# Kernel tuning notes

Hardware: AMD Instinct MI355X
Metric: run time of the kernel (lower is better)

Reference implementation:

```python
import jax, jax.numpy as jnp
import numpy as np

B, T, S = 128, 512, 30      # batch, input temporal length, sensor channels
F_NUM, KS, NL = 64, 5, 4    # conv filters, kernel size, n conv layers
H, NC = 128, 18             # GRU hidden dim, n classes


def setup_inputs() -> dict:
    key = jax.random.key(0)
    ks = jax.random.split(key, 16)
    r = lambda i, shape, s=0.05: (jax.random.normal(ks[i], shape, jnp.float32) * s)
    return {
        "x": jax.random.normal(ks[0], (B, 1, T, S), jnp.float32),
        "conv0_w": r(1, (F_NUM, 1, KS, 1), 0.2),          # first Conv2d (in=1)
        "convs_w": r(2, (3, F_NUM, F_NUM, KS, 1), 0.05),  # conv layers 1..3
        "conv_b": r(3, (NL, F_NUM)),
        "bn_gamma": jnp.ones((NL, F_NUM), jnp.float32),
        "bn_beta": jnp.zeros((NL, F_NUM), jnp.float32),
        "bn_mean": jnp.zeros((NL, F_NUM), jnp.float32),
        "bn_var": jnp.ones((NL, F_NUM), jnp.float32),
        "wq": r(4, (F_NUM, F_NUM), 0.1),
        "wk": r(5, (F_NUM, F_NUM), 0.1),
        "wv": r(6, (F_NUM, F_NUM), 0.1),
        "sa_gamma": jnp.array([0.1], jnp.float32),
        "fc1_w": r(7, (H, S * F_NUM), 0.02),
        "fc1_b": r(8, (H,)),
        "gru_wih": r(9, (2, 3 * H, H), 0.05),
        "gru_whh": r(10, (2, 3 * H, H), 0.05),
        "gru_bih": r(11, (2, 3 * H)),
        "gru_bhh": r(12, (2, 3 * H)),
        "pred_w": r(13, (NC, H), 0.05),
        "pred_b": r(14, (NC,)),
    }


def reference(x, conv0_w, convs_w, conv_b, bn_gamma, bn_beta, bn_mean, bn_var,
              wq, wk, wv, sa_gamma, fc1_w, fc1_b,
              gru_wih, gru_whh, gru_bih, gru_bhh, pred_w, pred_b):
    eps = 1e-5

    def conv_relu_bn(y, w, b, g, be, m, v):
        # Conv2d kernel (KS,1) stride (2,1), then ReLU, then BatchNorm (eval mode)
        y = jax.lax.conv_general_dilated(
            y, w, (2, 1), 'VALID',
            dimension_numbers=('NCHW', 'OIHW', 'NCHW')) + b[None, :, None, None]
        y = jax.nn.relu(y)
        inv = g / jnp.sqrt(v + eps)
        return y * inv[None, :, None, None] + (be - m * inv)[None, :, None, None]

    x = conv_relu_bn(x, conv0_w, conv_b[0], bn_gamma[0], bn_beta[0], bn_mean[0], bn_var[0])
    for i in range(3):  # fixed small layer loop
        x = conv_relu_bn(x, convs_w[i], conv_b[i + 1], bn_gamma[i + 1],
                         bn_beta[i + 1], bn_mean[i + 1], bn_var[i + 1])

    Bn, Fn, Ln, Sn = x.shape
    # Fold time into batch: per-timestep SelfAttention over (F, S) slices, vectorized
    xs = jnp.transpose(x, (0, 2, 1, 3)).reshape(Bn * Ln, Fn, Sn)  # (N, F, S)
    f = jnp.einsum('of,nfs->nos', wq, xs)   # query (1x1 conv1d, no bias)
    g = jnp.einsum('of,nfs->nos', wk, xs)   # key
    h = jnp.einsum('of,nfs->nos', wv, xs)   # value
    scores = jnp.einsum('noi,noj->nij', f, g)         # bmm(f^T, g): (N, S, S)
    beta = jax.nn.softmax(scores, axis=1)             # softmax over dim=1 (as torch)
    o = sa_gamma[0] * jnp.einsum('nfi,nij->nfj', h, beta) + xs  # (N, F, S)

    # cat over t then permute(0,3,1,2).reshape == (B, L, F*S)
    seq = o.reshape(Bn, Ln, Fn * Sn)
    seq = jax.nn.relu(seq @ fc1_w.T + fc1_b)          # (B, L, H); dropout = eval noop
    xs_t = jnp.transpose(seq, (1, 0, 2))              # (L, B, H) seq-first for GRU

    def gru_layer(xseq, wih, whh, bih, bhh):
        Hd = whh.shape[1]
        def step(hprev, xt):
            gi = xt @ wih.T + bih
            gh = hprev @ whh.T + bhh
            ir, iz, inn = jnp.split(gi, 3, axis=-1)
            hr, hz, hn = jnp.split(gh, 3, axis=-1)
            r = jax.nn.sigmoid(ir + hr)
            z = jax.nn.sigmoid(iz + hz)
            n = jnp.tanh(inn + r * hn)
            hnew = (1.0 - z) * n + z * hprev
            return hnew, hnew
        h0 = jnp.zeros((xseq.shape[1], Hd), xseq.dtype)
        _, ys = jax.lax.scan(step, h0, xseq)
        return ys

    for l in range(2):  # 2-layer GRU (inter-layer dropout = eval noop)
        xs_t = gru_layer(xs_t, gru_wih[l], gru_whh[l], gru_bih[l], gru_bhh[l])

    return xs_t[-1] @ pred_w.T + pred_b               # (B, NC)
```

## Files before the change

kernel.cpp:

```cpp
#include <hip/hip_runtime.h>
#include <math.h>

#define EPS 1e-5f

#define B_  128
#define T0_ 512
#define S_  30
#define F_  64
#define L1_ 254
#define L2_ 125
#define L3_ 61
#define L4_ 29
#define BS_ (B_*S_)
#define N_  (B_*L4_)
#define H_  128
#define NC_ 18
#define KFS 1920

typedef __attribute__((ext_vector_type(8))) short short8;
typedef __attribute__((ext_vector_type(16))) float f32x16;

__device__ __forceinline__ uint32_t f2bf(float f) {
    uint32_t u = __float_as_uint(f);
    return (u + 0x7fffu + ((u >> 16) & 1u)) >> 16;
}

typedef const __attribute__((address_space(1))) uint32_t* gas_t;
typedef __attribute__((address_space(3))) uint32_t* las_t;
__device__ __forceinline__ void glds16(const void* g, void* l) {
    __builtin_amdgcn_global_load_lds((gas_t)g, (las_t)l, 16, 0, 0);
}

#define MFMA(a,b,c) __builtin_amdgcn_mfma_f32_32x32x16_bf16(a, b, c, 0, 0, 0)

__global__ __launch_bounds__(256) void prepack_kernel(
    const float* __restrict__ wcs, ushort* __restrict__ aw)
{
    int i = blockIdx.x*256 + threadIdx.x;
    int l = i / 20480, r = i - l*20480;
    int j = r & 7, f = (r >> 3) & 63, g = r >> 9;
    int chalf = g & 1, ck = (g >> 1) & 3, kh = g >> 3;
    int c = ck*16 + chalf*8 + j;
    float w = wcs[l*20480 + f*320 + c*5 + kh];
    uint32_t h = f2bf(w);
    uint32_t lo = f2bf(w - __uint_as_float(h << 16));
    aw[l*40960 + r]         = (ushort)h;
    aw[l*40960 + 20480 + r] = (ushort)lo;
}

__device__ __forceinline__ f32x16 conv_mm(
    const ushort* __restrict__ Ash, const ushort* __restrict__ Bh,
    const ushort* __restrict__ Bl, int f0, int t0, int tcol, int chalf)
{
    f32x16 acc;
    #pragma unroll
    for (int i = 0; i < 16; i++) acc[i] = 0.f;
    int fa = (f0 + tcol)*8;
    int t = t0 + tcol;
    #pragma unroll
    for (int kh = 0; kh < 5; kh++) {
        int tp = 2*t + kh;
        int sw = (tp >> 3) & 7;
        const ushort* brh = Bh + tp*64;
        const ushort* brl = Bl + tp*64;
        #pragma unroll
        for (int ck = 0; ck < 4; ck++) {
            int g = (kh*4+ck)*2 + chalf;
            short8 AH = *(const short8*)(Ash + g*512 + fa);
            short8 AL = *(const short8*)(Ash + 20480 + g*512 + fa);
            int col = (((ck*2+chalf) ^ sw) << 3);
            short8 BH = *(const short8*)(brh + col);
            short8 BL = *(const short8*)(brl + col);
            acc = MFMA(AH, BH, acc);
            acc = MFMA(AH, BL, acc);
            acc = MFMA(AL, BH, acc);
        }
    }
    return acc;
}

__global__ __launch_bounds__(512) void conv01_mfma(
    const float* __restrict__ x,  const float* __restrict__ w0,
    const ushort* __restrict__ aw, const float* __restrict__ cb,
    const float* __restrict__ bg, const float* __restrict__ bb,
    const float* __restrict__ bm, const float* __restrict__ bv,
    char* __restrict__ y1h, char* __restrict__ y1l)
{
    __shared__ uint32_t Ash_w[20480];
    __shared__ ushort Yt[2][264*64];
    __shared__ float xl[T0_];
    int bs = blockIdx.x, b = bs/S_, s = bs - b*S_;
    int tid = threadIdx.x;
    #pragma unroll
    for (int k = 0; k < 10; k++)
        glds16((const char*)aw + k*8192 + tid*16, (char*)Ash_w + k*8192 + (tid>>6)*1024);
    xl[tid] = x[(b*T0_ + tid)*S_ + s];
    __syncthreads();
    {
        int c = tid & 63;
        float w00=w0[c*5], w01=w0[c*5+1], w02=w0[c*5+2], w03=w0[c*5+3], w04=w0[c*5+4];
        float bias = cb[c];
        float inv = bg[c]*rsqrtf(bv[c]+EPS);
        float add = bb[c]-bm[c]*inv;
        for (int tp = (tid>>6); tp < 264; tp += 8) {
            float val = 0.f;
            if (tp < L1_) {
                float a = bias + w00*xl[2*tp] + w01*xl[2*tp+1] + w02*xl[2*tp+2]
                               + w03*xl[2*tp+3] + w04*xl[2*tp+4];
                val = fmaxf(a, 0.f)*inv + add;
            }
            uint32_t h = f2bf(val);
            uint32_t l = f2bf(val - __uint_as_float(h<<16));
            int col = c ^ ((tp>>3 & 7) << 3);
            Yt[0][tp*64 + col] = (ushort)h;
            Yt[1][tp*64 + col] = (ushort)l;
        }
    }
    __syncthreads();
    int lane = tid & 63, wv = tid >> 6;
    int tcol = lane & 31, chalf = lane >> 5;
    int f0 = (wv>>2)*32, t0 = (wv&3)*32;
    f32x16 acc = conv_mm((const ushort*)Ash_w, Yt[0], Yt[1], f0, t0, tcol, chalf);
    __syncthreads();
    int t = t0 + tcol;
    if (t < L2_) {
        int swzo = ((t>>1) ^ (t>>3)) & 7;
        #pragma unroll
        for (int rq = 0; rq < 4; rq++) {
            int fb = f0 + 8*rq + 4*chalf;
            uint32_t h[4], l[4];
            #pragma unroll
            for (int j = 0; j < 4; j++) {
                int r = rq*4 + j, f = fb + j;
                float inv = bg[64+f]*rsqrtf(bv[64+f]+EPS);
                float val = fmaxf(acc[r]+cb[64+f], 0.f)*inv + (bb[64+f]-bm[64+f]*inv);
                h[j] = f2bf(val);
                l[j] = f2bf(val - __uint_as_float(h[j]<<16));
            }
            int pos = ((((fb>>3) ^ swzo) << 3) + (fb & 7));
            uint2 H; H.x = h[0] | (h[1]<<16); H.y = h[2] | (h[3]<<16);
            uint2 L; L.x = l[0] | (l[1]<<16); L.y = l[2] | (l[3]<<16);
            *(uint2*)&Yt[0][t*64 + pos] = H;
            *(uint2*)&Yt[1][t*64 + pos] = L;
        }
    }
    __syncthreads();
    for (int i = tid; i < 2000; i += 512) {
        int pl = i >= 1000, jj = pl ? i-1000 : i;
        int tr = jj >> 3, p = jj & 7;
        int q = p ^ ((tr>>1) & 7);
        uint4 v = *(const uint4*)&Yt[pl][tr*64 + q*8];
        *(uint4*)((pl ? y1l : y1h) + (size_t)bs*16000 + tr*128 + p*16) = v;
    }
}

__global__ __launch_bounds__(512) void conv2_mfma(
    const ushort* __restrict__ aw, const float* __restrict__ cb,
    const float* __restrict__ bg, const float* __restrict__ bb,
    const float* __restrict__ bm, const float* __restrict__ bv,
    char* __restrict__ yh, char* __restrict__ yl)
{
    __shared__ uint32_t Ash_w[20480];
    __shared__ ushort Yt[2][2][132*64];
    int bs0 = blockIdx.x*2, tid = threadIdx.x;
    const char* asrc = (const char*)aw + 81920;
    #pragma unroll
    for (int k = 0; k < 10; k++)
        glds16(asrc + k*8192 + tid*16, (char*)Ash_w + k*8192 + (tid>>6)*1024);
    #pragma unroll
    for (int sl = 0; sl < 2; sl++)
        #pragma unroll
        for (int pl = 0; pl < 2; pl++) {
            const char* src = (pl ? yl : yh) + (size_t)(bs0+sl)*16000;
            glds16(src + tid*16,        (char*)&Yt[sl][pl][0] + (tid>>6)*1024);
            glds16(src + 8192 + tid*16, (char*)&Yt[sl][pl][0] + 8192 + (tid>>6)*1024);
        }
    __syncthreads();
    for (int i = tid; i < 4*224; i += 512) {
        int g = i / 224, w2 = i - g*224;
        ((uint32_t*)&Yt[g>>1][g&1][125*64])[w2] = 0;
    }
    __syncthreads();
    int lane = tid & 63, wv = tid >> 6;
    int tcol = lane & 31, chalf = lane >> 5;
    int sl = wv >> 2, f0 = ((wv>>1)&1)*32, t0 = (wv&1)*32;
    f32x16 acc = conv_mm((const ushort*)Ash_w, Yt[sl][0], Yt[sl][1], f0, t0, tcol, chalf);
    __syncthreads();
    int t = t0 + tcol;
    if (t < L3_) {
        int swzo = ((t>>1) ^ (t>>3)) & 7;
        #pragma unroll
        for (int rq = 0; rq < 4; rq++) {
            int fb = f0 + 8*rq + 4*chalf;
            uint32_t h[4], l[4];
            #pragma unroll
            for (int j = 0; j < 4; j++) {
                int r = rq*4 + j, f = fb + j;
                float inv = bg[128+f]*rsqrtf(bv[128+f]+EPS);
                float val = fmaxf(acc[r]+cb[128+f], 0.f)*inv + (bb[128+f]-bm[128+f]*inv);
                h[j] = f2bf(val);
                l[j] = f2bf(val - __uint_as_float(h[j]<<16));
            }
            int pos = ((((fb>>3) ^ swzo) << 3) + (fb & 7));
            uint2 H; H.x = h[0] | (h[1]<<16); H.y = h[2] | (h[3]<<16);
            uint2 L; L.x = l[0] | (l[1]<<16); L.y = l[2] | (l[3]<<16);
            *(uint2*)&Yt[sl][0][t*64 + pos] = H;
            *(uint2*)&Yt[sl][1][t*64 + pos] = L;
        }
    }
    __syncthreads();
    for (int i = tid; i < 1952; i += 512) {
        int s2 = i / 976, r2 = i - s2*976;
        int pl = r2 >= 488, jj = pl ? r2-488 : r2;
        int tr = jj >> 3, p = jj & 7;
        int q = p ^ ((tr>>1) & 7);
        uint4 v = *(const uint4*)&Yt[s2][pl][tr*64 + q*8];
        *(uint4*)((pl ? yl : yh) + (size_t)(bs0+s2)*16000 + tr*128 + p*16) = v;
    }
}

__global__ __launch_bounds__(512) void conv3_mfma(
    const ushort* __restrict__ aw, const float* __restrict__ cb,
    const float* __restrict__ bg, const float* __restrict__ bb,
    const float* __restrict__ bm, const float* __restrict__ bv,
    const char* __restrict__ yh, const char* __restrict__ yl,
    float* __restrict__ y3)
{
    __shared__ uint32_t Ash_w[20480];
    __shared__ ushort Yt[4][2][68*64];
    int bs0 = blockIdx.x*4, tid = threadIdx.x;
    const char* asrc = (const char*)aw + 163840;
    #pragma unroll
    for (int k = 0; k < 10; k++)
        glds16(asrc + k*8192 + tid*16, (char*)Ash_w + k*8192 + (tid>>6)*1024);
    #pragma unroll
    for (int sl = 0; sl < 4; sl++)
        #pragma unroll
        for (int pl = 0; pl < 2; pl++) {
            const char* src = (pl ? yl : yh) + (size_t)(bs0+sl)*16000;
            glds16(src + tid*16, (char*)&Yt[sl][pl][0] + (tid>>6)*1024);
        }
    __syncthreads();
    for (int i = tid; i < 8*224; i += 512) {
        int g = i / 224, w2 = i - g*224;
        ((uint32_t*)&Yt[g>>1][g&1][61*64])[w2] = 0;
    }
    __syncthreads();
    int lane = tid & 63, wv = tid >> 6;
    int tcol = lane & 31, chalf = lane >> 5;
    int sl = wv >> 1, f0 = (wv&1)*32;
    f32x16 acc = conv_mm((const ushort*)Ash_w, Yt[sl][0], Yt[sl][1], f0, 0, tcol, chalf);
    int t = tcol;
    if (t < L4_) {
        #pragma unroll
        for (int r = 0; r < 16; r++) {
            int f = f0 + (r&3) + 8*(r>>2) + 4*chalf;
            float inv = bg[192+f]*rsqrtf(bv[192+f]+EPS);
            float val = fmaxf(acc[r]+cb[192+f], 0.f)*inv + (bb[192+f]-bm[192+f]*inv);
            y3[((size_t)(bs0+sl)*F_ + f)*L4_ + t] = val;
        }
    }
}

__global__ __launch_bounds__(256) void transp_kernel(
    const float* __restrict__ y3, float* __restrict__ xs)
{
    __shared__ float tl[15*F_*L4_];
    int b = blockIdx.x >> 1, s0 = (blockIdx.x & 1)*15;
    int tid = threadIdx.x;
    const float* src = y3 + (b*S_ + s0)*F_*L4_;
    for (int i = tid; i < 15*F_*L4_; i += 256) tl[i] = src[i];
    __syncthreads();
    for (int i = tid; i < L4_*F_*15; i += 256) {
        int l = i/(F_*15), f = (i/15)%F_, ss = i%15;
        xs[((b*L4_+l)*F_+f)*S_ + s0+ss] = tl[(ss*F_+f)*L4_ + l];
    }
}

__global__ __launch_bounds__(256) void attn_kernel(
    const float* __restrict__ xsg, const float* __restrict__ wq,
    const float* __restrict__ wk,  const float* __restrict__ wv,
    const float* __restrict__ gam, float* __restrict__ seq)
{
    __shared__ float X[F_][32];
    __shared__ float QKV[192][36];
    __shared__ float BETA[S_][36];
    int n = blockIdx.x, tid = threadIdx.x;
    for (int i = tid; i < KFS; i += 256) X[i/S_][i%S_] = xsg[n*KFS + i];
    for (int i = tid; i < 128; i += 256) X[i>>1][30 + (i&1)] = 0.f;
    __syncthreads();

    if (tid < 192) {
        int wsel = tid >> 6, row = tid & 63;
        const float* W = (wsel==0) ? wq : (wsel==1) ? wk : wv;
        float4 wr_[16];
        #pragma unroll
        for (int u = 0; u < 16; u++) wr_[u] = ((const float4*)(W + row*64))[u];
        float acc[32];
        #pragma unroll
        for (int i = 0; i < 32; i++) acc[i] = 0.f;
        #pragma unroll
        for (int u = 0; u < 16; u++) {
            float4 w4 = wr_[u];
            #pragma unroll
            for (int c = 0; c < 4; c++) {
                float wv_ = (c==0) ? w4.x : (c==1) ? w4.y : (c==2) ? w4.z : w4.w;
                const float4* xr = (const float4*)&X[u*4+c][0];
                #pragma unroll
                for (int q = 0; q < 8; q++) {
                    float4 xq = xr[q];
                    acc[q*4+0] += wv_*xq.x; acc[q*4+1] += wv_*xq.y;
                    acc[q*4+2] += wv_*xq.z; acc[q*4+3] += wv_*xq.w;
                }
            }
        }
        #pragma unroll
        for (int q = 0; q < 8; q++) {
            float4 o4; o4.x=acc[q*4]; o4.y=acc[q*4+1]; o4.z=acc[q*4+2]; o4.w=acc[q*4+3];
            *(float4*)&QKV[tid][q*4] = o4;
        }
    }
    __syncthreads();

    if (tid < 240) {
        int j = tid >> 3, iq = tid & 7;
        float4 s4 = {0.f, 0.f, 0.f, 0.f};
        for (int o = 0; o < 64; o++) {
            float4 q4 = *(const float4*)&QKV[o][iq*4];
            float kv = QKV[64+o][j];
            s4.x += q4.x*kv; s4.y += q4.y*kv; s4.z += q4.z*kv; s4.w += q4.w*kv;
        }
        if (iq == 7) { s4.z = -1e30f; s4.w = -1e30f; }
        float m = fmaxf(fmaxf(s4.x, s4.y), fmaxf(s4.z, s4.w));
        m = fmaxf(m, __shfl_xor(m, 1, 8));
        m = fmaxf(m, __shfl_xor(m, 2, 8));
        m = fmaxf(m, __shfl_xor(m, 4, 8));
        float e0 = expf(s4.x-m), e1 = expf(s4.y-m), e2 = expf(s4.z-m), e3 = expf(s4.w-m);
        if (iq == 7) { e2 = 0.f; e3 = 0.f; }
        float sum = e0+e1+e2+e3;
        sum += __shfl_xor(sum, 1, 8);
        sum += __shfl_xor(sum, 2, 8);
        sum += __shfl_xor(sum, 4, 8);
        float inv = 1.f/sum;
        int i0 = iq*4;
        BETA[i0][j]   = e0*inv;
        BETA[i0+1][j] = e1*inv;
        if (iq < 7) { BETA[i0+2][j] = e2*inv; BETA[i0+3][j] = e3*inv; }
    }
    __syncthreads();

    {
        int f = tid >> 2, jh = tid & 3;
        float acc[8];
        #pragma unroll
        for (int i = 0; i < 8; i++) acc[i] = 0.f;
        for (int i = 0; i < S_; i++) {
            float v = QKV[128+f][i];
            float4 b0 = *(const float4*)&BETA[i][jh*8];
            float4 b1 = *(const float4*)&BETA[i][jh*8+4];
            acc[0] += v*b0.x; acc[1] += v*b0.y; acc[2] += v*b0.z; acc[3] += v*b0.w;
            acc[4] += v*b1.x; acc[5] += v*b1.y; acc[6] += v*b1.z; acc[7] += v*b1.w;
        }
        float g = gam[0];
        int j0 = jh*8;
        #pragma unroll
        for (int jj = 0; jj < 8; jj++) {
            int j = j0 + jj;
            if (j < S_) seq[n*KFS + f*S_ + j] = g*acc[jj] + X[f][j];
        }
    }
}

__global__ __launch_bounds__(256) void fc1_kernel(
    const float* __restrict__ seq, const float* __restrict__ w,
    const float* __restrict__ bias, float* __restrict__ out)
{
    __shared__ float Sm[8*KFS];
    int n0 = blockIdx.x*8, tid = threadIdx.x;
    for (int i = tid; i < 8*KFS; i += 256) Sm[i] = seq[n0*KFS + i];
    __syncthreads();
    int h = tid & 127, rp = tid >> 7;
    float acc[4] = {0,0,0,0};
    const float4* wp = (const float4*)(w + h*KFS);
    #pragma unroll 4
    for (int k = 0; k < KFS/4; k++) {
        float4 wvv = wp[k];
        #pragma unroll
        for (int j = 0; j < 4; j++) {
            float4 sv = ((const float4*)&Sm[(rp*4+j)*KFS])[k];
            acc[j] += wvv.x*sv.x + wvv.y*sv.y + wvv.z*sv.z + wvv.w*sv.w;
        }
    }
    float bb2 = bias[h];
    #pragma unroll
    for (int j = 0; j < 4; j++)
        out[(n0 + rp*4 + j)*H_ + h] = fmaxf(acc[j] + bb2, 0.f);
}

__global__ __launch_bounds__(768) void gru_kernel(
    const float* __restrict__ xin,  const float* __restrict__ wih,
    const float* __restrict__ whh,  const float* __restrict__ bih,
    const float* __restrict__ bhh,  const float* __restrict__ pw,
    const float* __restrict__ pb,   float* __restrict__ out)
{
    __shared__ float xh[H_], hh[H_], gi[3*H_], gh[3*H_], ys[L4_][H_];
    int b = blockIdx.x, tid = threadIdx.x;
    int mat = tid / 384, j = tid % 384;
    float4 wr[32];
    for (int layer = 0; layer < 2; layer++) {
        const float* wsrc = (mat ? whh : wih) + layer*384*128 + j*128;
        #pragma unroll
        for (int u = 0; u < 32; u++) wr[u] = ((const float4*)wsrc)[u];
        float bias = (mat ? bhh : bih)[layer*384 + j];
        if (tid < H_) hh[tid] = 0.f;
        __syncthreads();
        for (int t = 0; t < L4_; t++) {
            if (tid < H_) xh[tid] = (layer == 0) ? xin[(b*L4_+t)*H_ + tid] : ys[t][tid];
            __syncthreads();
            const float* src = mat ? hh : xh;
            float a0=0,a1=0,a2=0,a3=0;
            #pragma unroll
            for (int u = 0; u < 32; u++) {
                float4 xv = ((const float4*)src)[u];
                a0 += wr[u].x*xv.x; a1 += wr[u].y*xv.y;
                a2 += wr[u].z*xv.z; a3 += wr[u].w*xv.w;
            }
            float g = (a0+a1)+(a2+a3) + bias;
            if (mat) gh[j] = g; else gi[j] = g;
            __syncthreads();
            if (tid < H_) {
                int m = tid;
                float r = 1.f/(1.f+expf(-(gi[m]      + gh[m])));
                float z = 1.f/(1.f+expf(-(gi[m+128]  + gh[m+128])));
                float n = tanhf(gi[m+256] + r*gh[m+256]);
                float hnew = (1.f-z)*n + z*hh[m];
                hh[m] = hnew; ys[t][m] = hnew;
            }
            __syncthreads();
        }
    }
    if (tid < NC_) {
        float a = pb[tid];
        for (int k = 0; k < H_; k++) a += pw[tid*H_+k]*hh[k];
        out[b*NC_ + tid] = a;
    }
}

extern "C" void kernel_launch(void* const* d_in, const int* in_sizes, int n_in,
                              void* d_out, int out_size, void* d_ws, size_t ws_size,
                              hipStream_t stream) {
    const float* x    = (const float*)d_in[0];
    const float* w0   = (const float*)d_in[1];
    const float* wcs  = (const float*)d_in[2];
    const float* cb   = (const float*)d_in[3];
    const float* bg   = (const float*)d_in[4];
    const float* bb   = (const float*)d_in[5];
    const float* bm   = (const float*)d_in[6];
    const float* bv   = (const float*)d_in[7];
    const float* wq   = (const float*)d_in[8];
    const float* wk   = (const float*)d_in[9];
    const float* wv   = (const float*)d_in[10];
    const float* gam  = (const float*)d_in[11];
    const float* fw   = (const float*)d_in[12];
    const float* fb   = (const float*)d_in[13];
    const float* gwih = (const float*)d_in[14];
    const float* gwhh = (const float*)d_in[15];
    const float* gbih = (const float*)d_in[16];
    const float* gbhh = (const float*)d_in[17];
    const float* pw   = (const float*)d_in[18];
    const float* pb   = (const float*)d_in[19];
    float* out = (float*)d_out;
    uint32_t* wsu = (uint32_t*)d_ws;

    ushort* aw  = (ushort*)wsu;
    char* y1h   = (char*)(wsu + 61440);
    char* y1l   = (char*)(wsu + 15425536);
    float* y3v  = (float*)(wsu + 30789632);
    float* seqv = (float*)(wsu + 30789632);
    float* xsv  = (float*)(wsu + 37916672);
    float* f1v  = (float*)(wsu + 37916672);

    prepack_kernel<<<240, 256, 0, stream>>>(wcs, aw);
    conv01_mfma<<<BS_, 512, 0, stream>>>(x, w0, aw, cb, bg, bb, bm, bv, y1h, y1l);
    conv2_mfma<<<BS_/2, 512, 0, stream>>>(aw, cb, bg, bb, bm, bv, y1h, y1l);
    conv3_mfma<<<BS_/4, 512, 0, stream>>>(aw, cb, bg, bb, bm, bv, y1h, y1l, y3v);
    transp_kernel<<<2*B_, 256, 0, stream>>>(y3v, xsv);
    attn_kernel<<<N_, 256, 0, stream>>>(xsv, wq, wk, wv, gam, seqv);
    fc1_kernel<<<N_/8, 256, 0, stream>>>(seqv, fw, fb, f1v);
    gru_kernel<<<B_, 768, 0, stream>>>(f1v, gwih, gwhh, gbih, gbhh, pw, pb, out);
}
```

Measured before the change: 720.0 us.

## Keep conv weights in registers and loop persistent blocks over multiple slices

The three MFMA conv kernels now load their bf16 hi/lo weight fragments once into registers instead of staging 80KB of weights in LDS per block. Each block then processes several (b,s) slices: 5 for conv01, 8 for conv2 and conv3, with double-buffered async global-to-LDS loads of the next slices in conv2 and conv3. BN epilogue constants are precomputed into shared memory, and the first-layer conv is vectorised over 4 channels per thread. The aim is to amortise weight loads and free LDS for 2 blocks per CU. The cost is high register pressure from 40 short8 fragments per thread, which could cause spills, and fewer blocks in the grid.

```diff
diff --git a/kernel.cpp b/kernel.cpp
--- a/kernel.cpp
+++ b/kernel.cpp
@@ -33,6 +33,8 @@
 
 #define MFMA(a,b,c) __builtin_amdgcn_mfma_f32_32x32x16_bf16(a, b, c, 0, 0, 0)
 
+union ABu { uint4 u; short8 s; };
+
 __global__ __launch_bounds__(256) void prepack_kernel(
     const float* __restrict__ wcs, ushort* __restrict__ aw)
 {
@@ -48,15 +50,26 @@
     aw[l*40960 + 20480 + r] = (ushort)lo;
 }
 
-__device__ __forceinline__ f32x16 conv_mm(
-    const ushort* __restrict__ Ash, const ushort* __restrict__ Bh,
-    const ushort* __restrict__ Bl, int f0, int t0, int tcol, int chalf)
+__device__ __forceinline__ void load_areg(const ushort* __restrict__ aw_l,
+                                          int f0, int tcol, int chalf,
+                                          ABu* AH_, ABu* AL_)
+{
+    #pragma unroll
+    for (int idx = 0; idx < 20; idx++) {
+        int r = (idx*2 + chalf)*512 + (f0 + tcol)*8;
+        AH_[idx].u = *(const uint4*)(aw_l + r);
+        AL_[idx].u = *(const uint4*)(aw_l + 20480 + r);
+    }
+}
+
+__device__ __forceinline__ f32x16 conv_mm_reg(
+    const ABu* AH_, const ABu* AL_,
+    const ushort* __restrict__ Bh, const ushort* __restrict__ Bl,
+    int t, int chalf)
 {
     f32x16 acc;
     #pragma unroll
     for (int i = 0; i < 16; i++) acc[i] = 0.f;
-    int fa = (f0 + tcol)*8;
-    int t = t0 + tcol;
     #pragma unroll
     for (int kh = 0; kh < 5; kh++) {
         int tp = 2*t + kh;
@@ -65,200 +78,276 @@
         const ushort* brl = Bl + tp*64;
         #pragma unroll
         for (int ck = 0; ck < 4; ck++) {
-            int g = (kh*4+ck)*2 + chalf;
-            short8 AH = *(const short8*)(Ash + g*512 + fa);
-            short8 AL = *(const short8*)(Ash + 20480 + g*512 + fa);
-            int col = (((ck*2+chalf) ^ sw) << 3);
+            int idx = kh*4 + ck;
+            int col = (((ck*2 + chalf) ^ sw) << 3);
             short8 BH = *(const short8*)(brh + col);
             short8 BL = *(const short8*)(brl + col);
-            acc = MFMA(AH, BH, acc);
-            acc = MFMA(AH, BL, acc);
-            acc = MFMA(AL, BH, acc);
+            acc = MFMA(AH_[idx].s, BH, acc);
+            acc = MFMA(AH_[idx].s, BL, acc);
+            acc = MFMA(AL_[idx].s, BH, acc);
         }
     }
     return acc;
 }
 
-__global__ __launch_bounds__(512) void conv01_mfma(
+__global__ __launch_bounds__(512, 2) void conv01_mfma(
     const float* __restrict__ x,  const float* __restrict__ w0,
     const ushort* __restrict__ aw, const float* __restrict__ cb,
     const float* __restrict__ bg, const float* __restrict__ bb,
     const float* __restrict__ bm, const float* __restrict__ bv,
     char* __restrict__ y1h, char* __restrict__ y1l)
 {
-    __shared__ uint32_t Ash_w[20480];
     __shared__ ushort Yt[2][264*64];
     __shared__ float xl[T0_];
-    int bs = blockIdx.x, b = bs/S_, s = bs - b*S_;
+    __shared__ float ep0[64], ep1[64], ep2[64];
     int tid = threadIdx.x;
-    #pragma unroll
-    for (int k = 0; k < 10; k++)
-        glds16((const char*)aw + k*8192 + tid*16, (char*)Ash_w + k*8192 + (tid>>6)*1024);
-    xl[tid] = x[(b*T0_ + tid)*S_ + s];
-    __syncthreads();
-    {
-        int c = tid & 63;
-        float w00=w0[c*5], w01=w0[c*5+1], w02=w0[c*5+2], w03=w0[c*5+3], w04=w0[c*5+4];
-        float bias = cb[c];
-        float inv = bg[c]*rsqrtf(bv[c]+EPS);
-        float add = bb[c]-bm[c]*inv;
-        for (int tp = (tid>>6); tp < 264; tp += 8) {
-            float val = 0.f;
-            if (tp < L1_) {
-                float a = bias + w00*xl[2*tp] + w01*xl[2*tp+1] + w02*xl[2*tp+2]
-                               + w03*xl[2*tp+3] + w04*xl[2*tp+4];
-                val = fmaxf(a, 0.f)*inv + add;
-            }
-            uint32_t h = f2bf(val);
-            uint32_t l = f2bf(val - __uint_as_float(h<<16));
-            int col = c ^ ((tp>>3 & 7) << 3);
-            Yt[0][tp*64 + col] = (ushort)h;
-            Yt[1][tp*64 + col] = (ushort)l;
-        }
-    }
-    __syncthreads();
     int lane = tid & 63, wv = tid >> 6;
     int tcol = lane & 31, chalf = lane >> 5;
-    int f0 = (wv>>2)*32, t0 = (wv&3)*32;
-    f32x16 acc = conv_mm((const ushort*)Ash_w, Yt[0], Yt[1], f0, t0, tcol, chalf);
-    __syncthreads();
-    int t = t0 + tcol;
-    if (t < L2_) {
-        int swzo = ((t>>1) ^ (t>>3)) & 7;
-        #pragma unroll
-        for (int rq = 0; rq < 4; rq++) {
-            int fb = f0 + 8*rq + 4*chalf;
-            uint32_t h[4], l[4];
-            #pragma unroll
-            for (int j = 0; j < 4; j++) {
-                int r = rq*4 + j, f = fb + j;
-                float inv = bg[64+f]*rsqrtf(bv[64+f]+EPS);
-                float val = fmaxf(acc[r]+cb[64+f], 0.f)*inv + (bb[64+f]-bm[64+f]*inv);
-                h[j] = f2bf(val);
-                l[j] = f2bf(val - __uint_as_float(h[j]<<16));
-            }
-            int pos = ((((fb>>3) ^ swzo) << 3) + (fb & 7));
-            uint2 H; H.x = h[0] | (h[1]<<16); H.y = h[2] | (h[3]<<16);
-            uint2 L; L.x = l[0] | (l[1]<<16); L.y = l[2] | (l[3]<<16);
-            *(uint2*)&Yt[0][t*64 + pos] = H;
-            *(uint2*)&Yt[1][t*64 + pos] = L;
-        }
-    }
-    __syncthreads();
-    for (int i = tid; i < 2000; i += 512) {
-        int pl = i >= 1000, jj = pl ? i-1000 : i;
-        int tr = jj >> 3, p = jj & 7;
-        int q = p ^ ((tr>>1) & 7);
-        uint4 v = *(const uint4*)&Yt[pl][tr*64 + q*8];
-        *(uint4*)((pl ? y1l : y1h) + (size_t)bs*16000 + tr*128 + p*16) = v;
-    }
-}
-
-__global__ __launch_bounds__(512) void conv2_mfma(
+    int f0 = (wv>>2)*32, t0 = (wv&3)*32, t = t0 + tcol;
+
+    ABu AH_[20], AL_[20];
+    load_areg(aw, f0, tcol, chalf, AH_, AL_);
+
+    int cq = tid & 15, tpb = tid >> 4, c0 = cq*4;
+    float w0r[20], inv0[4], add0[4], b0r[4];
+    #pragma unroll
+    for (int j = 0; j < 4; j++) {
+        int c = c0 + j;
+        #pragma unroll
+        for (int u = 0; u < 5; u++) w0r[j*5+u] = w0[c*5+u];
+        float iv = bg[c]*rsqrtf(bv[c]+EPS);
+        inv0[j] = iv; add0[j] = bb[c]-bm[c]*iv; b0r[j] = cb[c];
+    }
+    if (tid < 64) {
+        float iv = bg[64+tid]*rsqrtf(bv[64+tid]+EPS);
+        ep0[tid] = iv; ep1[tid] = bb[64+tid]-bm[64+tid]*iv; ep2[tid] = cb[64+tid];
+    }
+
+    for (int sl = 0; sl < 5; sl++) {
+        int bs = blockIdx.x*5 + sl, b = bs/S_, s = bs - b*S_;
+        xl[tid] = x[(b*T0_ + tid)*S_ + s];
+        __syncthreads();
+        #pragma unroll
+        for (int k = 0; k < 9; k++) {
+            int tp = tpb + k*32;
+            if (tp < 264) {
+                float v4[4];
+                if (tp < L1_) {
+                    float2 xa = *(const float2*)&xl[2*tp];
+                    float2 xb = *(const float2*)&xl[2*tp+2];
+                    float2 xc = *(const float2*)&xl[2*tp+4];
+                    #pragma unroll
+                    for (int j = 0; j < 4; j++) {
+                        float a = b0r[j] + w0r[j*5]*xa.x + w0r[j*5+1]*xa.y
+                                + w0r[j*5+2]*xb.x + w0r[j*5+3]*xb.y + w0r[j*5+4]*xc.x;
+                        v4[j] = fmaxf(a, 0.f)*inv0[j] + add0[j];
+                    }
+                } else { v4[0]=v4[1]=v4[2]=v4[3]=0.f; }
+                uint32_t h0=f2bf(v4[0]), h1=f2bf(v4[1]), h2=f2bf(v4[2]), h3=f2bf(v4[3]);
+                uint2 H; H.x = h0|(h1<<16); H.y = h2|(h3<<16);
+                uint2 L;
+                L.x = f2bf(v4[0]-__uint_as_float(h0<<16)) | (f2bf(v4[1]-__uint_as_float(h1<<16))<<16);
+                L.y = f2bf(v4[2]-__uint_as_float(h2<<16)) | (f2bf(v4[3]-__uint_as_float(h3<<16))<<16);
+                int pos = tp*64 + (c0 ^ (((tp>>3)&7)<<3));
+                *(uint2*)&Yt[0][pos] = H;
+                *(uint2*)&Yt[1][pos] = L;
+            }
+        }
+        __syncthreads();
+        f32x16 acc = conv_mm_reg(AH_, AL_, Yt[0], Yt[1], t, chalf);
+        __syncthreads();
+        if (t < L2_) {
+            int swzo = ((t>>1) ^ (t>>3)) & 7;
+            #pragma unroll
+            for (int rq = 0; rq < 4; rq++) {
+                int fb = f0 + 8*rq + 4*chalf;
+                uint32_t h[4], l[4];
+                #pragma unroll
+                for (int j = 0; j < 4; j++) {
+                    int r = rq*4 + j, f = fb + j;
+                    float val = fmaxf(acc[r]+ep2[f], 0.f)*ep0[f] + ep1[f];
+                    h[j] = f2bf(val);
+                    l[j] = f2bf(val - __uint_as_float(h[j]<<16));
+                }
+                int pos = ((((fb>>3) ^ swzo) << 3) + (fb & 7));
+                uint2 H; H.x = h[0] | (h[1]<<16); H.y = h[2] | (h[3]<<16);
+                uint2 L; L.x = l[0] | (l[1]<<16); L.y = l[2] | (l[3]<<16);
+                *(uint2*)&Yt[0][t*64 + pos] = H;
+                *(uint2*)&Yt[1][t*64 + pos] = L;
+            }
+        }
+        __syncthreads();
+        for (int i = tid; i < 2000; i += 512) {
+            int pl = i >= 1000, jj = pl ? i-1000 : i;
+            int tr = jj >> 3, p = jj & 7;
+            int q = p ^ ((tr>>1) & 7);
+            uint4 v = *(const uint4*)&Yt[pl][tr*64 + q*8];
+            *(uint4*)((pl ? y1l : y1h) + (size_t)bs*16000 + tr*128 + p*16) = v;
+        }
+    }
+}
+
+__global__ __launch_bounds__(512, 2) void conv2_mfma(
     const ushort* __restrict__ aw, const float* __restrict__ cb,
     const float* __restrict__ bg, const float* __restrict__ bb,
     const float* __restrict__ bm, const float* __restrict__ bv,
     char* __restrict__ yh, char* __restrict__ yl)
 {
-    __shared__ uint32_t Ash_w[20480];
-    __shared__ ushort Yt[2][2][132*64];
-    int bs0 = blockIdx.x*2, tid = threadIdx.x;
-    const char* asrc = (const char*)aw + 81920;
-    #pragma unroll
-    for (int k = 0; k < 10; k++)
-        glds16(asrc + k*8192 + tid*16, (char*)Ash_w + k*8192 + (tid>>6)*1024);
-    #pragma unroll
-    for (int sl = 0; sl < 2; sl++)
-        #pragma unroll
-        for (int pl = 0; pl < 2; pl++) {
-            const char* src = (pl ? yl : yh) + (size_t)(bs0+sl)*16000;
-            glds16(src + tid*16,        (char*)&Yt[sl][pl][0] + (tid>>6)*1024);
-            glds16(src + 8192 + tid*16, (char*)&Yt[sl][pl][0] + 8192 + (tid>>6)*1024);
-        }
-    __syncthreads();
-    for (int i = tid; i < 4*224; i += 512) {
-        int g = i / 224, w2 = i - g*224;
-        ((uint32_t*)&Yt[g>>1][g&1][125*64])[w2] = 0;
-    }
-    __syncthreads();
+    __shared__ ushort Yt[2][2][2][132*64];
+    __shared__ float ep0[64], ep1[64], ep2[64];
+    int tid = threadIdx.x;
     int lane = tid & 63, wv = tid >> 6;
     int tcol = lane & 31, chalf = lane >> 5;
-    int sl = wv >> 2, f0 = ((wv>>1)&1)*32, t0 = (wv&1)*32;
-    f32x16 acc = conv_mm((const ushort*)Ash_w, Yt[sl][0], Yt[sl][1], f0, t0, tcol, chalf);
-    __syncthreads();
-    int t = t0 + tcol;
-    if (t < L3_) {
-        int swzo = ((t>>1) ^ (t>>3)) & 7;
-        #pragma unroll
-        for (int rq = 0; rq < 4; rq++) {
-            int fb = f0 + 8*rq + 4*chalf;
-            uint32_t h[4], l[4];
-            #pragma unroll
-            for (int j = 0; j < 4; j++) {
-                int r = rq*4 + j, f = fb + j;
-                float inv = bg[128+f]*rsqrtf(bv[128+f]+EPS);
-                float val = fmaxf(acc[r]+cb[128+f], 0.f)*inv + (bb[128+f]-bm[128+f]*inv);
-                h[j] = f2bf(val);
-                l[j] = f2bf(val - __uint_as_float(h[j]<<16));
-            }
-            int pos = ((((fb>>3) ^ swzo) << 3) + (fb & 7));
-            uint2 H; H.x = h[0] | (h[1]<<16); H.y = h[2] | (h[3]<<16);
-            uint2 L; L.x = l[0] | (l[1]<<16); L.y = l[2] | (l[3]<<16);
-            *(uint2*)&Yt[sl][0][t*64 + pos] = H;
-            *(uint2*)&Yt[sl][1][t*64 + pos] = L;
-        }
-    }
-    __syncthreads();
-    for (int i = tid; i < 1952; i += 512) {
-        int s2 = i / 976, r2 = i - s2*976;
-        int pl = r2 >= 488, jj = pl ? r2-488 : r2;
-        int tr = jj >> 3, p = jj & 7;
-        int q = p ^ ((tr>>1) & 7);
-        uint4 v = *(const uint4*)&Yt[s2][pl][tr*64 + q*8];
-        *(uint4*)((pl ? yl : yh) + (size_t)(bs0+s2)*16000 + tr*128 + p*16) = v;
-    }
-}
-
-__global__ __launch_bounds__(512) void conv3_mfma(
+    int slw = wv >> 2, f0 = ((wv>>1)&1)*32, t0 = (wv&1)*32, t = t0 + tcol;
+    int blk = blockIdx.x;
+
+    ABu AH_[20], AL_[20];
+    load_areg(aw + 40960, f0, tcol, chalf, AH_, AL_);
+    if (tid < 64) {
+        float iv = bg[128+tid]*rsqrtf(bv[128+tid]+EPS);
+        ep0[tid] = iv; ep1[tid] = bb[128+tid]-bm[128+tid]*iv; ep2[tid] = cb[128+tid];
+    }
+    #pragma unroll
+    for (int sl2 = 0; sl2 < 2; sl2++)
+        #pragma unroll
+        for (int pl = 0; pl < 2; pl++) {
+            const char* src = (pl ? yl : yh) + (size_t)(blk*8 + sl2)*16000;
+            glds16(src + tid*16,        (char*)&Yt[0][sl2][pl][0] + (tid>>6)*1024);
+            glds16(src + 8192 + tid*16, (char*)&Yt[0][sl2][pl][0] + 8192 + (tid>>6)*1024);
+        }
+    for (int i = tid; i < 1024; i += 512) {
+        int g = i >> 7, w2 = i & 127;
+        ((uint32_t*)&Yt[g>>2][(g>>1)&1][g&1][128*64])[w2] = 0;
+    }
+    __syncthreads();
+    for (int i = tid; i < 384; i += 512) {
+        int g = i / 96, w2 = i - g*96;
+        ((uint32_t*)&Yt[0][g>>1][g&1][125*64])[w2] = 0;
+    }
+    __syncthreads();
+
+    for (int it = 0; it < 4; it++) {
+        int buf = it & 1;
+        int bs0 = blk*8 + it*2;
+        if (it < 3) {
+            #pragma unroll
+            for (int sl2 = 0; sl2 < 2; sl2++)
+                #pragma unroll
+                for (int pl = 0; pl < 2; pl++) {
+                    const char* src = (pl ? yl : yh) + (size_t)(bs0 + 2 + sl2)*16000;
+                    glds16(src + tid*16,        (char*)&Yt[buf^1][sl2][pl][0] + (tid>>6)*1024);
+                    glds16(src + 8192 + tid*16, (char*)&Yt[buf^1][sl2][pl][0] + 8192 + (tid>>6)*1024);
+                }
+        }
+        f32x16 acc = conv_mm_reg(AH_, AL_, Yt[buf][slw][0], Yt[buf][slw][1], t, chalf);
+        __syncthreads();
+        if (it < 3) {
+            for (int i = tid; i < 384; i += 512) {
+                int g = i / 96, w2 = i - g*96;
+                ((uint32_t*)&Yt[buf^1][g>>1][g&1][125*64])[w2] = 0;
+            }
+        }
+        if (t < L3_) {
+            int swzo = ((t>>1) ^ (t>>3)) & 7;
+            #pragma unroll
+            for (int rq = 0; rq < 4; rq++) {
+                int fb = f0 + 8*rq + 4*chalf;
+                uint32_t h[4], l[4];
+                #pragma unroll
+                for (int j = 0; j < 4; j++) {
+                    int r = rq*4 + j, f = fb + j;
+                    float val = fmaxf(acc[r]+ep2[f], 0.f)*ep0[f] + ep1[f];
+                    h[j] = f2bf(val);
+                    l[j] = f2bf(val - __uint_as_float(h[j]<<16));
+                }
+                int pos = ((((fb>>3) ^ swzo) << 3) + (fb & 7));
+                uint2 H; H.x = h[0] | (h[1]<<16); H.y = h[2] | (h[3]<<16);
+                uint2 L; L.x = l[0] | (l[1]<<16); L.y = l[2] | (l[3]<<16);
+                *(uint2*)&Yt[buf][slw][0][t*64 + pos] = H;
+                *(uint2*)&Yt[buf][slw][1][t*64 + pos] = L;
+            }
+        }
+        __syncthreads();
+        for (int i = tid; i < 1952; i += 512) {
+            int s2 = i / 976, r2 = i - s2*976;
+            int pl = r2 >= 488, jj = pl ? r2-488 : r2;
+            int tr = jj >> 3, p = jj & 7;
+            int q = p ^ ((tr>>1) & 7);
+            uint4 v = *(const uint4*)&Yt[buf][s2][pl][tr*64 + q*8];
+            *(uint4*)((pl ? yl : yh) + (size_t)(bs0+s2)*16000 + tr*128 + p*16) = v;
+        }
+        __syncthreads();
+    }
+}
+
+__global__ __launch_bounds__(512, 2) void conv3_mfma(
     const ushort* __restrict__ aw, const float* __restrict__ cb,
     const float* __restrict__ bg, const float* __restrict__ bb,
     const float* __restrict__ bm, const float* __restrict__ bv,
     const char* __restrict__ yh, const char* __restrict__ yl,
     float* __restrict__ y3)
 {
-    __shared__ uint32_t Ash_w[20480];
-    __shared__ ushort Yt[4][2][68*64];
-    int bs0 = blockIdx.x*4, tid = threadIdx.x;
-    const char* asrc = (const char*)aw + 163840;
-    #pragma unroll
-    for (int k = 0; k < 10; k++)
-        glds16(asrc + k*8192 + tid*16, (char*)Ash_w + k*8192 + (tid>>6)*1024);
-    #pragma unroll
-    for (int sl = 0; sl < 4; sl++)
-        #pragma unroll
-        for (int pl = 0; pl < 2; pl++) {
-            const char* src = (pl ? yl : yh) + (size_t)(bs0+sl)*16000;
-            glds16(src + tid*16, (char*)&Yt[sl][pl][0] + (tid>>6)*1024);
-        }
-    __syncthreads();
-    for (int i = tid; i < 8*224; i += 512) {
-        int g = i / 224, w2 = i - g*224;
-        ((uint32_t*)&Yt[g>>1][g&1][61*64])[w2] = 0;
-    }
-    __syncthreads();
+    __shared__ ushort Yt[2][4][2][68*64];
+    __shared__ float ep0[64], ep1[64], ep2[64];
+    int tid = threadIdx.x;
     int lane = tid & 63, wv = tid >> 6;
     int tcol = lane & 31, chalf = lane >> 5;
-    int sl = wv >> 1, f0 = (wv&1)*32;
-    f32x16 acc = conv_mm((const ushort*)Ash_w, Yt[sl][0], Yt[sl][1], f0, 0, tcol, chalf);
-    int t = tcol;
-    if (t < L4_) {
-        #pragma unroll
-        for (int r = 0; r < 16; r++) {
-            int f = f0 + (r&3) + 8*(r>>2) + 4*chalf;
-            float inv = bg[192+f]*rsqrtf(bv[192+f]+EPS);
-            float val = fmaxf(acc[r]+cb[192+f], 0.f)*inv + (bb[192+f]-bm[192+f]*inv);
-            y3[((size_t)(bs0+sl)*F_ + f)*L4_ + t] = val;
-        }
+    int slq = wv >> 1, f0 = (wv&1)*32, t = tcol;
+    int blk = blockIdx.x;
+
+    ABu AH_[20], AL_[20];
+    load_areg(aw + 81920, f0, tcol, chalf, AH_, AL_);
+    if (tid < 64) {
+        float iv = bg[192+tid]*rsqrtf(bv[192+tid]+EPS);
+        ep0[tid] = iv; ep1[tid] = bb[192+tid]-bm[192+tid]*iv; ep2[tid] = cb[192+tid];
+    }
+    #pragma unroll
+    for (int sl2 = 0; sl2 < 4; sl2++)
+        #pragma unroll
+        for (int pl = 0; pl < 2; pl++) {
+            const char* src = (pl ? yl : yh) + (size_t)(blk*8 + sl2)*16000;
+            glds16(src + tid*16, (char*)&Yt[0][sl2][pl][0] + (tid>>6)*1024);
+        }
+    for (int i = tid; i < 2048; i += 512) {
+        int g = i >> 7, w2 = i & 127;
+        ((uint32_t*)&Yt[g>>3][(g>>1)&3][g&1][64*64])[w2] = 0;
+    }
+    __syncthreads();
+    for (int i = tid; i < 768; i += 512) {
+        int g = i / 96, w2 = i - g*96;
+        ((uint32_t*)&Yt[0][g>>1][g&1][61*64])[w2] = 0;
+    }
+    __syncthreads();
+
+    for (int it = 0; it < 2; it++) {
+        int buf = it & 1;
+        int bs0 = blk*8 + it*4;
+        if (it < 1) {
+            #pragma unroll
+            for (int sl2 = 0; sl2 < 4; sl2++)
+                #pragma unroll
+                for (int pl = 0; pl < 2; pl++) {
+                    const char* src = (pl ? yl : yh) + (size_t)(bs0 + 4 + sl2)*16000;
+                    glds16(src + tid*16, (char*)&Yt[buf^1][sl2][pl][0] + (tid>>6)*1024);
+                }
+        }
+        f32x16 acc = conv_mm_reg(AH_, AL_, Yt[buf][slq][0], Yt[buf][slq][1], t, chalf);
+        if (t < L4_) {
+            #pragma unroll
+            for (int r = 0; r < 16; r++) {
+                int f = f0 + (r&3) + 8*(r>>2) + 4*chalf;
+                float val = fmaxf(acc[r]+ep2[f], 0.f)*ep0[f] + ep1[f];
+                y3[((size_t)(bs0+slq)*F_ + f)*L4_ + t] = val;
+            }
+        }
+        __syncthreads();
+        if (it < 1) {
+            for (int i = tid; i < 768; i += 512) {
+                int g = i / 96, w2 = i - g*96;
+                ((uint32_t*)&Yt[buf^1][g>>1][g&1][61*64])[w2] = 0;
+            }
+        }
+        __syncthreads();
     }
 }
 
@@ -289,7 +378,6 @@
     for (int i = tid; i < KFS; i += 256) X[i/S_][i%S_] = xsg[n*KFS + i];
     for (int i = tid; i < 128; i += 256) X[i>>1][30 + (i&1)] = 0.f;
     __syncthreads();
-
     if (tid < 192) {
         int wsel = tid >> 6, row = tid & 63;
         const float* W = (wsel==0) ? wq : (wsel==1) ? wk : wv;
@@ -321,7 +409,6 @@
         }
     }
     __syncthreads();
-
     if (tid < 240) {
         int j = tid >> 3, iq = tid & 7;
         float4 s4 = {0.f, 0.f, 0.f, 0.f};
@@ -348,7 +435,6 @@
         if (iq < 7) { BETA[i0+2][j] = e2*inv; BETA[i0+3][j] = e3*inv; }
     }
     __syncthreads();
-
     {
         int f = tid >> 2, jh = tid & 3;
         float acc[8];
@@ -481,9 +567,9 @@
     float* f1v  = (float*)(wsu + 37916672);
 
     prepack_kernel<<<240, 256, 0, stream>>>(wcs, aw);
-    conv01_mfma<<<BS_, 512, 0, stream>>>(x, w0, aw, cb, bg, bb, bm, bv, y1h, y1l);
-    conv2_mfma<<<BS_/2, 512, 0, stream>>>(aw, cb, bg, bb, bm, bv, y1h, y1l);
-    conv3_mfma<<<BS_/4, 512, 0, stream>>>(aw, cb, bg, bb, bm, bv, y1h, y1l, y3v);
+    conv01_mfma<<<768, 512, 0, stream>>>(x, w0, aw, cb, bg, bb, bm, bv, y1h, y1l);
+    conv2_mfma<<<480, 512, 0, stream>>>(aw, cb, bg, bb, bm, bv, y1h, y1l);
+    conv3_mfma<<<480, 512, 0, stream>>>(aw, cb, bg, bb, bm, bv, y1h, y1l, y3v);
     transp_kernel<<<2*B_, 256, 0, stream>>>(y3v, xsv);
     attn_kernel<<<N_, 256, 0, stream>>>(xsv, wq, wk, wv, gam, seqv);
     fc1_kernel<<<N_/8, 256, 0, stream>>>(seqv, fw, fb, f1v);
```

Result: no change. 726.7 us (+0.9%).
